# Optimization experiments

Hardware: AMD Instinct MI355X
Metric: run time of the kernel (lower is better)

The kernel has to match this reference:

```python
import jax, jax.numpy as jnp
import numpy as np
import math

B, A, IN_C, OUT_C = 64, 128, 128, 64

def _l2norm(x, eps=1e-12):
    # matches F.normalize(dim=1) on 2D input: x / max(||x||_2, eps) along last dim
    n = jnp.sqrt(jnp.sum(x * x, axis=-1, keepdims=True))
    return x / jnp.maximum(n, eps)

def setup_inputs() -> dict:
    key = jax.random.key(0)
    ks = jax.random.split(key, 7)
    s = 1.0 / math.sqrt(IN_C)
    return {
        "features": jax.random.normal(ks[0], (B, IN_C, A), dtype=jnp.float32),
        "Wq": jax.random.uniform(ks[1], (OUT_C, IN_C), jnp.float32, -s, s),
        "bq": jax.random.uniform(ks[2], (OUT_C,), jnp.float32, -s, s),
        "Wk": jax.random.uniform(ks[3], (OUT_C, IN_C), jnp.float32, -s, s),
        "bk": jax.random.uniform(ks[4], (OUT_C,), jnp.float32, -s, s),
        "Wv": jax.random.uniform(ks[5], (OUT_C, IN_C), jnp.float32, -s, s),
        "bv": jax.random.uniform(ks[6], (OUT_C,), jnp.float32, -s, s),
    }

def reference(features, Wq, bq, Wk, bk, Wv, bv):
    b = features.shape[0]
    f = jnp.transpose(features, (0, 2, 1))          # (b, a, in_c)
    a = f.shape[1]
    q = f @ Wq.T + bq                               # (b, a, d)
    k = f @ Wk.T + bk
    v = f @ Wv.T + bv
    d = q.shape[-1]
    qf = q.reshape(-1, d)                           # (N, d), N = b*a
    kf = k.reshape(-1, d)
    vf = v.reshape(-1, d)
    att = jax.nn.softmax(qf @ kf.T / math.sqrt(d), axis=1)  # (N, N)
    qkv = att @ vf                                  # (N, d)
    qkv_n = _l2norm(qkv).reshape(b, a, d)
    v_n = _l2norm(vf).reshape(b, a, d)
    # sim_s[i,j] = (1/a) * sum_t v_n[i,t] . qkv_n[j,t]  (diagonal-trace over 'a')
    sim_s = jnp.einsum('bad,cad->bc', v_n, qkv_n) / a
    return sim_s
```

## Files before the change

### kernel.cpp

```cpp
#include <hip/hip_runtime.h>
#include <hip/hip_bf16.h>

#define NROW 8192
#define INC  128
#define OUTC 64
#define BG   16

#define QSCALE 0.18033688011112042f

typedef __bf16 bf16x8 __attribute__((ext_vector_type(8)));
typedef __bf16 bf16x4 __attribute__((ext_vector_type(4)));
typedef short  s16x4  __attribute__((ext_vector_type(4)));
typedef float  f32x4  __attribute__((ext_vector_type(4)));

static __device__ __forceinline__ f32x4 mfma16(bf16x8 a, bf16x8 b, f32x4 c) {
    return __builtin_amdgcn_mfma_f32_16x16x32_bf16(a, b, c, 0, 0, 0);
}
static __device__ __forceinline__ f32x4 mfma1k(s16x4 a, s16x4 b, f32x4 c) {
    return __builtin_amdgcn_mfma_f32_16x16x16bf16_1k(a, b, c, 0, 0, 0);
}

static __device__ __forceinline__ bf16x8 cvt8(float4 lo, float4 hi) {
    bf16x8 r;
    r[0] = (__bf16)lo.x; r[1] = (__bf16)lo.y; r[2] = (__bf16)lo.z; r[3] = (__bf16)lo.w;
    r[4] = (__bf16)hi.x; r[5] = (__bf16)hi.y; r[6] = (__bf16)hi.z; r[7] = (__bf16)hi.w;
    return r;
}

__global__ __launch_bounds__(256) void proj_kernel(
    const float* __restrict__ feat,
    const float* __restrict__ Wq, const float* __restrict__ bq,
    const float* __restrict__ Wk, const float* __restrict__ bk,
    const float* __restrict__ Wv, const float* __restrict__ bv,
    __hip_bfloat16* __restrict__ qbf, __hip_bfloat16* __restrict__ kbf,
    __hip_bfloat16* __restrict__ vbf, __hip_bfloat16* __restrict__ vnb)
{
    __shared__ float slab[32 * 132];
    __shared__ float vbuf[32 * 66];
    __shared__ float invb[32];

    const int blk = blockIdx.x;
    const int mat = blk >> 8;
    const int b   = (blk >> 2) & 63;
    const int a0  = (blk & 3) * 32;
    const int r0  = b * 128 + a0;
    const float* fb = feat + (size_t)b * INC * 128;

    for (int i = threadIdx.x; i < 32 * 128; i += 256) {
        int c = i >> 5, a = i & 31;
        slab[a * 132 + c] = fb[c * 128 + a0 + a];
    }
    __syncthreads();

    const int w    = threadIdx.x >> 6;
    const int lane = threadIdx.x & 63;
    const int l16  = lane & 15;
    const int quad = lane >> 4;
    const int n0   = w * 16;

    const float* W    = (mat == 0) ? Wq : (mat == 1) ? Wk : Wv;
    const float* bias = (mat == 0) ? bq : (mat == 1) ? bk : bv;

    f32x4 acc[2] = {{0.f,0.f,0.f,0.f},{0.f,0.f,0.f,0.f}};
    #pragma unroll
    for (int kc = 0; kc < 4; ++kc) {
        const int k0 = kc * 32 + quad * 8;
        const float* wr = W + (n0 + l16) * INC + k0;
        bf16x8 bfr = cvt8(*(const float4*)wr, *(const float4*)(wr + 4));
        #pragma unroll
        for (int u = 0; u < 2; ++u) {
            const float* ar = slab + (u * 16 + l16) * 132 + k0;
            bf16x8 afr = cvt8(*(const float4*)ar, *(const float4*)(ar + 4));
            acc[u] = mfma16(afr, bfr, acc[u]);
        }
    }
    const float bl = bias[n0 + l16];
    const float sc = (mat == 0) ? QSCALE : 1.0f;

    if (mat < 2) {
        __hip_bfloat16* dst = mat ? kbf : qbf;
        #pragma unroll
        for (int u = 0; u < 2; ++u) {
            const int base = ((((r0 >> 4) + u) * 4 + w) << 8) + l16;
            #pragma unroll
            for (int r = 0; r < 4; ++r)
                dst[base + (quad * 4 + r) * 16] = __float2bfloat16((acc[u][r] + bl) * sc);
        }
    } else {
        #pragma unroll
        for (int u = 0; u < 2; ++u)
            #pragma unroll
            for (int r = 0; r < 4; ++r)
                vbuf[(u * 16 + quad * 4 + r) * 66 + n0 + l16] = acc[u][r] + bl;
        __syncthreads();
        const int rl = threadIdx.x >> 3;
        const int jj = threadIdx.x & 7;
        float ss = 0.f;
        #pragma unroll
        for (int i = 0; i < 8; ++i) {
            float x = vbuf[rl * 66 + jj * 8 + i];
            ss += x * x;
        }
        ss += __shfl_xor(ss, 1, 64);
        ss += __shfl_xor(ss, 2, 64);
        ss += __shfl_xor(ss, 4, 64);
        if (jj == 0) invb[rl] = rsqrtf(fmaxf(ss, 1e-24f));
        __syncthreads();
        float inv = invb[rl];
        bf16x8 vp;
        #pragma unroll
        for (int i = 0; i < 8; ++i)
            vp[i] = (__bf16)(vbuf[rl * 66 + jj * 8 + i] * inv);
        *(bf16x8*)(vnb + (size_t)(r0 + rl) * 64 + jj * 8) = vp;
        const int tl = threadIdx.x & 15;
        const int n  = (threadIdx.x >> 4) & 3;
        const int s_ = threadIdx.x >> 6;
        bf16x8 pack;
        #pragma unroll
        for (int j = 0; j < 8; ++j) {
            int key = s_ * 8 + j;
            pack[j] = (__bf16)(vbuf[key * 66 + n * 16 + tl] * invb[key]);
        }
        const int base = ((((r0 >> 4) + (s_ >> 1)) * 4 + n) << 8) + tl * 16 + (s_ & 1) * 8;
        *(bf16x8*)(vbf + base) = pack;
    }
}

__global__ __launch_bounds__(256, 4) void attn_kernel(
    const __hip_bfloat16* __restrict__ qbf,
    const __hip_bfloat16* __restrict__ kbf,
    const __hip_bfloat16* __restrict__ vbf,
    float* __restrict__ Opart, float* __restrict__ lpart)
{
    const int qb    = blockIdx.x >> 4;
    const int bg    = blockIdx.x & 15;
    const int w     = threadIdx.x >> 6;
    const int lane  = threadIdx.x & 63;
    const int l16   = lane & 15;
    const int quad  = lane >> 4;
    const int r0    = qb * 128 + w * 32;
    const int fo    = l16 * 16 + quad * 4;
    const int fo32  = l16 * 16 + (quad & 1) * 8;
    const int qh    = quad >> 1;

    bf16x8 qf32[2][2];
    #pragma unroll
    for (int u = 0; u < 2; ++u)
        #pragma unroll
        for (int p = 0; p < 2; ++p)
            qf32[u][p] = *(const bf16x8*)(qbf +
                ((((r0 >> 4) + u) * 4 + p * 2 + qh) << 8) + fo32);

    f32x4 of[2][4];
    float lp[2] = {0.f, 0.f};
    #pragma unroll
    for (int u = 0; u < 2; ++u)
        #pragma unroll
        for (int n = 0; n < 4; ++n)
            of[u][n] = (f32x4){0.f, 0.f, 0.f, 0.f};

    const int ck0 = bg * 32;
    const char* kp = (const char*)kbf + ck0 * 2048 + qh * 512 + fo32 * 2;
    const char* vp = (const char*)vbf + ck0 * 2048 + fo * 2;

    bf16x8 kfA[2][2], kfB[2][2];
    #pragma unroll
    for (int h = 0; h < 2; ++h)
        #pragma unroll
        for (int p = 0; p < 2; ++p)
            kfA[h][p] = *(const bf16x8*)(kp + h * 2048 + p * 1024);
    kp += 4096;

    #pragma unroll 1
    for (int body = 0; body < 8; ++body) {
        #pragma unroll
        for (int st = 0; st < 2; ++st) {
            bf16x8 (&kf)[2][2] = (st == 0) ? kfA : kfB;
            bf16x8 (&kn)[2][2] = (st == 0) ? kfB : kfA;
            s16x4 vf[4][2];
            #pragma unroll
            for (int n = 0; n < 4; ++n)
                #pragma unroll
                for (int h = 0; h < 2; ++h)
                    vf[n][h] = *(const s16x4*)(vp + h * 2048 + n * 512);
            #pragma unroll
            for (int h = 0; h < 2; ++h)
                #pragma unroll
                for (int p = 0; p < 2; ++p)
                    kn[h][p] = *(const bf16x8*)(kp + h * 2048 + p * 1024);
            vp += 4096;
            kp += 4096;

            const f32x4 zero = (f32x4){0.f, 0.f, 0.f, 0.f};
            #pragma unroll
            for (int u = 0; u < 2; ++u) {
                f32x4 s0 = mfma16(kf[0][0], qf32[u][0], zero);
                s0       = mfma16(kf[0][1], qf32[u][1], s0);
                f32x4 s1 = mfma16(kf[1][0], qf32[u][0], zero);
                s1       = mfma16(kf[1][1], qf32[u][1], s1);
                union { bf16x4 v; s16x4 s; } pf0, pf1;
                #pragma unroll
                for (int r = 0; r < 4; ++r) {
                    float p0 = __builtin_amdgcn_exp2f(s0[r]);
                    float p1 = __builtin_amdgcn_exp2f(s1[r]);
                    lp[0 + u] += p0 + p1;
                    pf0.v[r] = (__bf16)p0;
                    pf1.v[r] = (__bf16)p1;
                }
                #pragma unroll
                for (int n = 0; n < 4; ++n) {
                    of[u][n] = mfma1k(pf0.s, vf[n][0], of[u][n]);
                    of[u][n] = mfma1k(pf1.s, vf[n][1], of[u][n]);
                }
            }
        }
    }

    #pragma unroll
    for (int u = 0; u < 2; ++u) {
        float v = lp[u];
        v += __shfl_xor(v, 16, 64);
        v += __shfl_xor(v, 32, 64);
        lp[u] = v;
    }

    const int task = (qb * 4 + w) * 16 + bg;
    float* Ob = Opart + (size_t)task * 2048;
    #pragma unroll
    for (int u = 0; u < 2; ++u)
        #pragma unroll
        for (int n = 0; n < 4; ++n)
            #pragma unroll
            for (int r = 0; r < 4; ++r)
                Ob[(u * 16 + quad * 4 + r) * 64 + n * 16 + l16] = of[u][n][r];
    if (quad == 0) {
        lpart[task * 32 + l16]      = lp[0];
        lpart[task * 32 + 16 + l16] = lp[1];
    }
}

__global__ __launch_bounds__(256) void combine_kernel(
    const float* __restrict__ Opart, const float* __restrict__ lpart,
    __hip_bfloat16* __restrict__ qnb)
{
    const int r    = blockIdx.x * 4 + (threadIdx.x >> 6);
    const int c    = threadIdx.x & 63;
    const int tile = r >> 5, row = r & 31;
    float acc = 0.f, lsum = 0.f;
    #pragma unroll
    for (int g = 0; g < 16; ++g) {
        int task = tile * 16 + g;
        acc  += Opart[(size_t)task * 2048 + row * 64 + c];
        lsum += lpart[task * 32 + row];
    }
    float q = acc / lsum;
    float ss = q * q;
    ss += __shfl_xor(ss, 1, 64);
    ss += __shfl_xor(ss, 2, 64);
    ss += __shfl_xor(ss, 4, 64);
    ss += __shfl_xor(ss, 8, 64);
    ss += __shfl_xor(ss, 16, 64);
    ss += __shfl_xor(ss, 32, 64);
    qnb[(size_t)r * 64 + c] = __float2bfloat16(q * rsqrtf(fmaxf(ss, 1e-24f)));
}

__global__ __launch_bounds__(256) void sim_kernel(
    const __hip_bfloat16* __restrict__ vnb,
    const __hip_bfloat16* __restrict__ qnb,
    float* __restrict__ out)
{
    const int w    = threadIdx.x >> 6;
    const int lane = threadIdx.x & 63;
    const int l16  = lane & 15;
    const int quad = lane >> 4;
    const int kblk = blockIdx.x * 256;

    f32x4 acc[4][4];
    #pragma unroll
    for (int mi = 0; mi < 4; ++mi)
        #pragma unroll
        for (int ni = 0; ni < 4; ++ni)
            acc[mi][ni] = (f32x4){0.f, 0.f, 0.f, 0.f};

    #pragma unroll
    for (int s = 0; s < 2; ++s) {
        const int ks = w * 2 + s;
        const int k0 = kblk + ks * 32 + quad * 8;
        bf16x8 af[4], bfv[4];
        #pragma unroll
        for (int mi = 0; mi < 4; ++mi)
            af[mi] = *(const bf16x8*)(vnb + (size_t)(mi * 16 + l16) * 8192 + k0);
        #pragma unroll
        for (int ni = 0; ni < 4; ++ni)
            bfv[ni] = *(const bf16x8*)(qnb + (size_t)(ni * 16 + l16) * 8192 + k0);
        #pragma unroll
        for (int mi = 0; mi < 4; ++mi)
            #pragma unroll
            for (int ni = 0; ni < 4; ++ni)
                acc[mi][ni] = mfma16(af[mi], bfv[ni], acc[mi][ni]);
    }

    #pragma unroll
    for (int mi = 0; mi < 4; ++mi)
        #pragma unroll
        for (int ni = 0; ni < 4; ++ni)
            #pragma unroll
            for (int r = 0; r < 4; ++r)
                atomicAdd(&out[(mi * 16 + quad * 4 + r) * 64 + ni * 16 + l16],
                          acc[mi][ni][r] * (1.f / 128.f));
}

extern "C" void kernel_launch(void* const* d_in, const int* in_sizes, int n_in,
                              void* d_out, int out_size, void* d_ws, size_t ws_size,
                              hipStream_t stream)
{
    const float* feat = (const float*)d_in[0];
    const float* Wq   = (const float*)d_in[1];
    const float* bq   = (const float*)d_in[2];
    const float* Wk   = (const float*)d_in[3];
    const float* bk   = (const float*)d_in[4];
    const float* Wv   = (const float*)d_in[5];
    const float* bv   = (const float*)d_in[6];
    float* out = (float*)d_out;

    const size_t MB = 1u << 20;
    char* ws = (char*)d_ws;
    __hip_bfloat16* qbf = (__hip_bfloat16*)(ws);
    __hip_bfloat16* kbf = (__hip_bfloat16*)(ws + 1 * MB);
    __hip_bfloat16* vbf = (__hip_bfloat16*)(ws + 2 * MB);
    __hip_bfloat16* vnb = (__hip_bfloat16*)(ws + 3 * MB);
    float* Opart = (float*)(ws + 4 * MB);
    float* lpart = (float*)(ws + 36 * MB);
    __hip_bfloat16* qnb = (__hip_bfloat16*)(ws + 37 * MB);

    (void)hipMemsetAsync(out, 0, 64 * 64 * sizeof(float), stream);
    proj_kernel<<<768, 256, 0, stream>>>(feat, Wq, bq, Wk, bk, Wv, bv, qbf, kbf, vbf, vnb);
    attn_kernel<<<1024, 256, 0, stream>>>(qbf, kbf, vbf, Opart, lpart);
    combine_kernel<<<2048, 256, 0, stream>>>(Opart, lpart, qnb);
    sim_kernel<<<32, 256, 0, stream>>>(vnb, qnb, out);
}
```

Baseline: 125.7 us.

## Replace split-K partial buffers with atomic accumulation and fuse combine into sim

```diff
diff --git a/kernel.cpp b/kernel.cpp
--- a/kernel.cpp
+++ b/kernel.cpp
@@ -33,13 +33,21 @@
     const float* __restrict__ Wk, const float* __restrict__ bk,
     const float* __restrict__ Wv, const float* __restrict__ bv,
     __hip_bfloat16* __restrict__ qbf, __hip_bfloat16* __restrict__ kbf,
-    __hip_bfloat16* __restrict__ vbf, __hip_bfloat16* __restrict__ vnb)
+    __hip_bfloat16* __restrict__ vbf, __hip_bfloat16* __restrict__ vnb,
+    float* __restrict__ Oacc )
 {
     __shared__ float slab[32 * 132];
     __shared__ float vbuf[32 * 66];
     __shared__ float invb[32];
 
     const int blk = blockIdx.x;
+
+    {
+        const int zi = blk * 256 + threadIdx.x;
+        if (zi < 133120)
+            ((float4*)Oacc)[zi] = (float4){0.f, 0.f, 0.f, 0.f};
+    }
+
     const int mat = blk >> 8;
     const int b   = (blk >> 2) & 63;
     const int a0  = (blk & 3) * 32;
@@ -130,8 +138,15 @@
     const __hip_bfloat16* __restrict__ qbf,
     const __hip_bfloat16* __restrict__ kbf,
     const __hip_bfloat16* __restrict__ vbf,
-    float* __restrict__ Opart, float* __restrict__ lpart)
+    float* __restrict__ Oacc, float* __restrict__ lacc,
+    float* __restrict__ outz)
 {
+    if (blockIdx.x == 0) {
+        #pragma unroll
+        for (int z = 0; z < 4; ++z)
+            ((float4*)outz)[threadIdx.x * 4 + z] = (float4){0.f, 0.f, 0.f, 0.f};
+    }
+
     const int qb    = blockIdx.x >> 4;
     const int bg    = blockIdx.x & 15;
     const int w     = threadIdx.x >> 6;
@@ -224,51 +239,54 @@
         lp[u] = v;
     }
 
-    const int task = (qb * 4 + w) * 16 + bg;
-    float* Ob = Opart + (size_t)task * 2048;
     #pragma unroll
     for (int u = 0; u < 2; ++u)
         #pragma unroll
         for (int n = 0; n < 4; ++n)
             #pragma unroll
             for (int r = 0; r < 4; ++r)
-                Ob[(u * 16 + quad * 4 + r) * 64 + n * 16 + l16] = of[u][n][r];
+                atomicAdd(&Oacc[(size_t)(r0 + u * 16 + quad * 4 + r) * 64 + n * 16 + l16],
+                          of[u][n][r]);
     if (quad == 0) {
-        lpart[task * 32 + l16]      = lp[0];
-        lpart[task * 32 + 16 + l16] = lp[1];
-    }
-}
-
-__global__ __launch_bounds__(256) void combine_kernel(
-    const float* __restrict__ Opart, const float* __restrict__ lpart,
-    __hip_bfloat16* __restrict__ qnb)
-{
-    const int r    = blockIdx.x * 4 + (threadIdx.x >> 6);
-    const int c    = threadIdx.x & 63;
-    const int tile = r >> 5, row = r & 31;
-    float acc = 0.f, lsum = 0.f;
-    #pragma unroll
-    for (int g = 0; g < 16; ++g) {
-        int task = tile * 16 + g;
-        acc  += Opart[(size_t)task * 2048 + row * 64 + c];
-        lsum += lpart[task * 32 + row];
-    }
-    float q = acc / lsum;
-    float ss = q * q;
-    ss += __shfl_xor(ss, 1, 64);
-    ss += __shfl_xor(ss, 2, 64);
-    ss += __shfl_xor(ss, 4, 64);
-    ss += __shfl_xor(ss, 8, 64);
-    ss += __shfl_xor(ss, 16, 64);
-    ss += __shfl_xor(ss, 32, 64);
-    qnb[(size_t)r * 64 + c] = __float2bfloat16(q * rsqrtf(fmaxf(ss, 1e-24f)));
+        atomicAdd(&lacc[r0 + l16],      lp[0]);
+        atomicAdd(&lacc[r0 + 16 + l16], lp[1]);
+    }
 }
 
 __global__ __launch_bounds__(256) void sim_kernel(
     const __hip_bfloat16* __restrict__ vnb,
-    const __hip_bfloat16* __restrict__ qnb,
+    const float* __restrict__ Oacc, const float* __restrict__ lacc,
     float* __restrict__ out)
 {
+    __shared__ __hip_bfloat16 qn[64][264];
+
+    const int a0 = blockIdx.x * 4;
+    {
+        const int i   = threadIdx.x;
+        const int b   = i >> 2, j = i & 3;
+        const int row = b * 128 + a0 + j;
+        const float4* Or = (const float4*)(Oacc + (size_t)row * 64);
+        const float inv_l = 1.0f / lacc[row];
+        float4 v[16];
+        float ss = 0.f;
+        #pragma unroll
+        for (int c4 = 0; c4 < 16; ++c4) {
+            float4 t = Or[c4];
+            t.x *= inv_l; t.y *= inv_l; t.z *= inv_l; t.w *= inv_l;
+            ss += t.x * t.x + t.y * t.y + t.z * t.z + t.w * t.w;
+            v[c4] = t;
+        }
+        const float inv = rsqrtf(fmaxf(ss, 1e-24f));
+        #pragma unroll
+        for (int c4 = 0; c4 < 16; ++c4) {
+            v[c4].x *= inv; v[c4].y *= inv; v[c4].z *= inv; v[c4].w *= inv;
+        }
+        #pragma unroll
+        for (int m = 0; m < 8; ++m)
+            *(bf16x8*)&qn[b][j * 64 + m * 8] = cvt8(v[2 * m], v[2 * m + 1]);
+    }
+    __syncthreads();
+
     const int w    = threadIdx.x >> 6;
     const int lane = threadIdx.x & 63;
     const int l16  = lane & 15;
@@ -284,15 +302,14 @@
 
     #pragma unroll
     for (int s = 0; s < 2; ++s) {
-        const int ks = w * 2 + s;
-        const int k0 = kblk + ks * 32 + quad * 8;
+        const int k0 = (w * 2 + s) * 32 + quad * 8;
         bf16x8 af[4], bfv[4];
         #pragma unroll
         for (int mi = 0; mi < 4; ++mi)
-            af[mi] = *(const bf16x8*)(vnb + (size_t)(mi * 16 + l16) * 8192 + k0);
+            af[mi] = *(const bf16x8*)(vnb + (size_t)(mi * 16 + l16) * 8192 + kblk + k0);
         #pragma unroll
         for (int ni = 0; ni < 4; ++ni)
-            bfv[ni] = *(const bf16x8*)(qnb + (size_t)(ni * 16 + l16) * 8192 + k0);
+            bfv[ni] = *(const bf16x8*)&qn[ni * 16 + l16][k0];
         #pragma unroll
         for (int mi = 0; mi < 4; ++mi)
             #pragma unroll
@@ -329,13 +346,11 @@
     __hip_bfloat16* kbf = (__hip_bfloat16*)(ws + 1 * MB);
     __hip_bfloat16* vbf = (__hip_bfloat16*)(ws + 2 * MB);
     __hip_bfloat16* vnb = (__hip_bfloat16*)(ws + 3 * MB);
-    float* Opart = (float*)(ws + 4 * MB);
-    float* lpart = (float*)(ws + 36 * MB);
-    __hip_bfloat16* qnb = (__hip_bfloat16*)(ws + 37 * MB);
-
-    (void)hipMemsetAsync(out, 0, 64 * 64 * sizeof(float), stream);
-    proj_kernel<<<768, 256, 0, stream>>>(feat, Wq, bq, Wk, bk, Wv, bv, qbf, kbf, vbf, vnb);
-    attn_kernel<<<1024, 256, 0, stream>>>(qbf, kbf, vbf, Opart, lpart);
-    combine_kernel<<<2048, 256, 0, stream>>>(Opart, lpart, qnb);
-    sim_kernel<<<32, 256, 0, stream>>>(vnb, qnb, out);
-}
+    float* Oacc = (float*)(ws + 4 * MB);
+    float* lacc = (float*)(ws + 6 * MB);
+
+    proj_kernel<<<768, 256, 0, stream>>>(feat, Wq, bq, Wk, bk, Wv, bv,
+                                         qbf, kbf, vbf, vnb, Oacc);
+    attn_kernel<<<1024, 256, 0, stream>>>(qbf, kbf, vbf, Oacc, lacc, out);
+    sim_kernel<<<32, 256, 0, stream>>>(vnb, Oacc, lacc, out);
+}
```

New measurement: 135.1 us. +7.5%, slower.

## Double query rows per wave in attention kernel to reuse K/V fragments

Applied to the files above, without the earlier changes.

```diff
diff --git a/kernel.cpp b/kernel.cpp
--- a/kernel.cpp
+++ b/kernel.cpp
@@ -126,7 +126,51 @@
     }
 }
 
-__global__ __launch_bounds__(256, 4) void attn_kernel(
+#define ATTN_ITER(K00,K01,K10,K11, NK00,NK01,NK10,NK11,                      \
+                  V0,V1,V2,V3,V4,V5,V6,V7,                                   \
+                  NV0,NV1,NV2,NV3,NV4,NV5,NV6,NV7)                           \
+    do {                                                                     \
+        NV0 = *(const s16x4*)(vp);                                           \
+        NV1 = *(const s16x4*)(vp + 512);                                     \
+        NV2 = *(const s16x4*)(vp + 1024);                                    \
+        NV3 = *(const s16x4*)(vp + 1536);                                    \
+        NV4 = *(const s16x4*)(vp + 2048);                                    \
+        NV5 = *(const s16x4*)(vp + 2560);                                    \
+        NV6 = *(const s16x4*)(vp + 3072);                                    \
+        NV7 = *(const s16x4*)(vp + 3584);                                    \
+        NK00 = *(const bf16x8*)(kp);                                         \
+        NK01 = *(const bf16x8*)(kp + 1024);                                  \
+        NK10 = *(const bf16x8*)(kp + 2048);                                  \
+        NK11 = *(const bf16x8*)(kp + 3072);                                  \
+        vp += 4096; kp += 4096;                                              \
+        const f32x4 zero = (f32x4){0.f, 0.f, 0.f, 0.f};                      \
+        _Pragma("unroll")                                                    \
+        for (int u = 0; u < 4; ++u) {                                        \
+            f32x4 s0 = mfma16(K00, qf32[u][0], zero);                        \
+            s0       = mfma16(K01, qf32[u][1], s0);                          \
+            f32x4 s1 = mfma16(K10, qf32[u][0], zero);                        \
+            s1       = mfma16(K11, qf32[u][1], s1);                          \
+            union { bf16x4 v; s16x4 s; } pf0, pf1;                           \
+            _Pragma("unroll")                                                \
+            for (int r = 0; r < 4; ++r) {                                    \
+                float p0 = __builtin_amdgcn_exp2f(s0[r]);                    \
+                float p1 = __builtin_amdgcn_exp2f(s1[r]);                    \
+                lp[u] += p0 + p1;                                            \
+                pf0.v[r] = (__bf16)p0;                                       \
+                pf1.v[r] = (__bf16)p1;                                       \
+            }                                                                \
+            of[u][0] = mfma1k(pf0.s, V0, of[u][0]);                          \
+            of[u][0] = mfma1k(pf1.s, V4, of[u][0]);                          \
+            of[u][1] = mfma1k(pf0.s, V1, of[u][1]);                          \
+            of[u][1] = mfma1k(pf1.s, V5, of[u][1]);                          \
+            of[u][2] = mfma1k(pf0.s, V2, of[u][2]);                          \
+            of[u][2] = mfma1k(pf1.s, V6, of[u][2]);                          \
+            of[u][3] = mfma1k(pf0.s, V3, of[u][3]);                          \
+            of[u][3] = mfma1k(pf1.s, V7, of[u][3]);                          \
+        }                                                                    \
+    } while (0)
+
+__global__ __launch_bounds__(256, 2) void attn_kernel(
     const __hip_bfloat16* __restrict__ qbf,
     const __hip_bfloat16* __restrict__ kbf,
     const __hip_bfloat16* __restrict__ vbf,
@@ -138,23 +182,23 @@
     const int lane  = threadIdx.x & 63;
     const int l16   = lane & 15;
     const int quad  = lane >> 4;
-    const int r0    = qb * 128 + w * 32;
+    const int r0    = qb * 256 + w * 64;
     const int fo    = l16 * 16 + quad * 4;
     const int fo32  = l16 * 16 + (quad & 1) * 8;
     const int qh    = quad >> 1;
 
-    bf16x8 qf32[2][2];
-    #pragma unroll
-    for (int u = 0; u < 2; ++u)
+    bf16x8 qf32[4][2];
+    #pragma unroll
+    for (int u = 0; u < 4; ++u)
         #pragma unroll
         for (int p = 0; p < 2; ++p)
             qf32[u][p] = *(const bf16x8*)(qbf +
                 ((((r0 >> 4) + u) * 4 + p * 2 + qh) << 8) + fo32);
 
-    f32x4 of[2][4];
-    float lp[2] = {0.f, 0.f};
-    #pragma unroll
-    for (int u = 0; u < 2; ++u)
+    f32x4 of[4][4];
+    float lp[4] = {0.f, 0.f, 0.f, 0.f};
+    #pragma unroll
+    for (int u = 0; u < 4; ++u)
         #pragma unroll
         for (int n = 0; n < 4; ++n)
             of[u][n] = (f32x4){0.f, 0.f, 0.f, 0.f};
@@ -163,61 +207,36 @@
     const char* kp = (const char*)kbf + ck0 * 2048 + qh * 512 + fo32 * 2;
     const char* vp = (const char*)vbf + ck0 * 2048 + fo * 2;
 
-    bf16x8 kfA[2][2], kfB[2][2];
-    #pragma unroll
-    for (int h = 0; h < 2; ++h)
-        #pragma unroll
-        for (int p = 0; p < 2; ++p)
-            kfA[h][p] = *(const bf16x8*)(kp + h * 2048 + p * 1024);
-    kp += 4096;
+    bf16x8 kA00, kA01, kA10, kA11, kB00, kB01, kB10, kB11;
+    s16x4  vA0, vA1, vA2, vA3, vA4, vA5, vA6, vA7;
+    s16x4  vB0, vB1, vB2, vB3, vB4, vB5, vB6, vB7;
+
+    vA0 = *(const s16x4*)(vp);
+    vA1 = *(const s16x4*)(vp + 512);
+    vA2 = *(const s16x4*)(vp + 1024);
+    vA3 = *(const s16x4*)(vp + 1536);
+    vA4 = *(const s16x4*)(vp + 2048);
+    vA5 = *(const s16x4*)(vp + 2560);
+    vA6 = *(const s16x4*)(vp + 3072);
+    vA7 = *(const s16x4*)(vp + 3584);
+    kA00 = *(const bf16x8*)(kp);
+    kA01 = *(const bf16x8*)(kp + 1024);
+    kA10 = *(const bf16x8*)(kp + 2048);
+    kA11 = *(const bf16x8*)(kp + 3072);
+    vp += 4096; kp += 4096;
 
     #pragma unroll 1
     for (int body = 0; body < 8; ++body) {
-        #pragma unroll
-        for (int st = 0; st < 2; ++st) {
-            bf16x8 (&kf)[2][2] = (st == 0) ? kfA : kfB;
-            bf16x8 (&kn)[2][2] = (st == 0) ? kfB : kfA;
-            s16x4 vf[4][2];
-            #pragma unroll
-            for (int n = 0; n < 4; ++n)
-                #pragma unroll
-                for (int h = 0; h < 2; ++h)
-                    vf[n][h] = *(const s16x4*)(vp + h * 2048 + n * 512);
-            #pragma unroll
-            for (int h = 0; h < 2; ++h)
-                #pragma unroll
-                for (int p = 0; p < 2; ++p)
-                    kn[h][p] = *(const bf16x8*)(kp + h * 2048 + p * 1024);
-            vp += 4096;
-            kp += 4096;
-
-            const f32x4 zero = (f32x4){0.f, 0.f, 0.f, 0.f};
-            #pragma unroll
-            for (int u = 0; u < 2; ++u) {
-                f32x4 s0 = mfma16(kf[0][0], qf32[u][0], zero);
-                s0       = mfma16(kf[0][1], qf32[u][1], s0);
-                f32x4 s1 = mfma16(kf[1][0], qf32[u][0], zero);
-                s1       = mfma16(kf[1][1], qf32[u][1], s1);
-                union { bf16x4 v; s16x4 s; } pf0, pf1;
-                #pragma unroll
-                for (int r = 0; r < 4; ++r) {
-                    float p0 = __builtin_amdgcn_exp2f(s0[r]);
-                    float p1 = __builtin_amdgcn_exp2f(s1[r]);
-                    lp[0 + u] += p0 + p1;
-                    pf0.v[r] = (__bf16)p0;
-                    pf1.v[r] = (__bf16)p1;
-                }
-                #pragma unroll
-                for (int n = 0; n < 4; ++n) {
-                    of[u][n] = mfma1k(pf0.s, vf[n][0], of[u][n]);
-                    of[u][n] = mfma1k(pf1.s, vf[n][1], of[u][n]);
-                }
-            }
-        }
-    }
-
-    #pragma unroll
-    for (int u = 0; u < 2; ++u) {
+        ATTN_ITER(kA00, kA01, kA10, kA11, kB00, kB01, kB10, kB11,
+                  vA0, vA1, vA2, vA3, vA4, vA5, vA6, vA7,
+                  vB0, vB1, vB2, vB3, vB4, vB5, vB6, vB7);
+        ATTN_ITER(kB00, kB01, kB10, kB11, kA00, kA01, kA10, kA11,
+                  vB0, vB1, vB2, vB3, vB4, vB5, vB6, vB7,
+                  vA0, vA1, vA2, vA3, vA4, vA5, vA6, vA7);
+    }
+
+    #pragma unroll
+    for (int u = 0; u < 4; ++u) {
         float v = lp[u];
         v += __shfl_xor(v, 16, 64);
         v += __shfl_xor(v, 32, 64);
@@ -225,17 +244,18 @@
     }
 
     const int task = (qb * 4 + w) * 16 + bg;
-    float* Ob = Opart + (size_t)task * 2048;
-    #pragma unroll
-    for (int u = 0; u < 2; ++u)
+    float* Ob = Opart + (size_t)task * 4096;
+    #pragma unroll
+    for (int u = 0; u < 4; ++u)
         #pragma unroll
         for (int n = 0; n < 4; ++n)
             #pragma unroll
             for (int r = 0; r < 4; ++r)
                 Ob[(u * 16 + quad * 4 + r) * 64 + n * 16 + l16] = of[u][n][r];
     if (quad == 0) {
-        lpart[task * 32 + l16]      = lp[0];
-        lpart[task * 32 + 16 + l16] = lp[1];
+        #pragma unroll
+        for (int u = 0; u < 4; ++u)
+            lpart[task * 64 + u * 16 + l16] = lp[u];
     }
 }
 
@@ -245,13 +265,13 @@
 {
     const int r    = blockIdx.x * 4 + (threadIdx.x >> 6);
     const int c    = threadIdx.x & 63;
-    const int tile = r >> 5, row = r & 31;
+    const int tile = r >> 6, row = r & 63;
     float acc = 0.f, lsum = 0.f;
     #pragma unroll
     for (int g = 0; g < 16; ++g) {
         int task = tile * 16 + g;
-        acc  += Opart[(size_t)task * 2048 + row * 64 + c];
-        lsum += lpart[task * 32 + row];
+        acc  += Opart[(size_t)task * 4096 + row * 64 + c];
+        lsum += lpart[task * 64 + row];
     }
     float q = acc / lsum;
     float ss = q * q;
@@ -335,7 +355,7 @@
 
     (void)hipMemsetAsync(out, 0, 64 * 64 * sizeof(float), stream);
     proj_kernel<<<768, 256, 0, stream>>>(feat, Wq, bq, Wk, bk, Wv, bv, qbf, kbf, vbf, vnb);
-    attn_kernel<<<1024, 256, 0, stream>>>(qbf, kbf, vbf, Opart, lpart);
+    attn_kernel<<<512, 256, 0, stream>>>(qbf, kbf, vbf, Opart, lpart);
     combine_kernel<<<2048, 256, 0, stream>>>(Opart, lpart, qnb);
     sim_kernel<<<32, 256, 0, stream>>>(vnb, qnb, out);
 }
```

After: 119.0 us. 5.3% less time.
